# Performance work log

Hardware: AMD Instinct MI355X
Metric: run time of the kernel (lower is better)

Reference implementation:

```python
import math
import jax, jax.numpy as jnp
import numpy as np

B, L, D, H = 4, 512, 256, 8
DH = D // H
BUCKETS = 11  # rel_pos_buckets; padding_idx = BUCKETS


def setup_inputs() -> dict:
    key = jax.random.key(0)
    ks = jax.random.split(key, 12)
    s = 0.02
    rel_table = jax.random.normal(ks[10], (BUCKETS + 1, D), dtype=jnp.float32) * s
    rel_table = rel_table.at[BUCKETS].set(0.0)  # padding_idx row is zero
    return {
        "inputs": jax.random.normal(ks[0], (B, L, D), dtype=jnp.float32),
        "mask": jax.random.randint(ks[1], (B, L, L), 0, 2) > 0,
        "distances": jax.random.randint(ks[2], (B, L, L), 0, BUCKETS + 1),
        "Wq": jax.random.normal(ks[3], (D, D), dtype=jnp.float32) * s,
        "bq": jnp.zeros((D,), jnp.float32),
        "Wk": jax.random.normal(ks[4], (D, D), dtype=jnp.float32) * s,
        "bk": jnp.zeros((D,), jnp.float32),
        "Wv": jax.random.normal(ks[5], (D, D), dtype=jnp.float32) * s,
        "bv": jnp.zeros((D,), jnp.float32),
        "Wo": jax.random.normal(ks[6], (D, D), dtype=jnp.float32) * s,
        "bo": jnp.zeros((D,), jnp.float32),
        "rel_table": rel_table,
        "u": jax.random.normal(ks[7], (D,), dtype=jnp.float32) * s,
        "v": jax.random.normal(ks[8], (D,), dtype=jnp.float32) * s,
    }


def reference(inputs, mask, distances, Wq, bq, Wk, bk, Wv, bv, Wo, bo, rel_table, u, v):
    def shape(x):  # (B, L, D) -> (B, H, L, DH)
        return x.reshape(B, L, H, DH).transpose(0, 2, 1, 3)

    q = shape(inputs @ Wq + bq) / math.sqrt(DH)
    k = shape(inputs @ Wk + bk)
    val = shape(inputs @ Wv + bv)

    # content term: (q + u) k^T
    a_c = jnp.einsum("bhqd,bhkd->bhqk", q + u.reshape(1, H, 1, DH), k)

    # relative-position term: embedding gather (padding row already zero, mask anyway)
    valid = (distances != BUCKETS)[..., None].astype(rel_table.dtype)
    rel = (rel_table[distances] * valid).reshape(B, L, L, H, DH)  # (B, Lq, Lk, H, DH)
    b_d = jnp.einsum("bhqd,bqkhd->bhqk", q + v.reshape(1, H, 1, DH), rel)

    scores = jnp.where(mask[:, None, :, :], jnp.float32(-1e18), a_c + b_d)
    attn = jax.nn.softmax(scores, axis=-1)  # (B, H, Lq, Lk)

    ctx = jnp.einsum("bhqk,bhkd->bhqd", attn, val)
    ctx = ctx.transpose(0, 2, 1, 3).reshape(B, L, D)
    output = ctx @ Wo + bo
    return output, attn
```

## Files before the change

### kernel.cpp

```cpp
#include <hip/hip_runtime.h>
#include <math.h>

#define BB 4
#define LL 512
#define DD 256
#define HH 8
#define DHH 32
#define NB 12

__global__ __launch_bounds__(256) void qkv_kernel(const float* __restrict__ x,
    const float* __restrict__ Wq, const float* __restrict__ bq,
    const float* __restrict__ Wk, const float* __restrict__ bk,
    const float* __restrict__ Wv, const float* __restrict__ bv,
    const float* __restrict__ uvec, const float* __restrict__ vvec,
    float* __restrict__ Qu, float* __restrict__ Qv,
    float* __restrict__ KT, float* __restrict__ V) {
    __shared__ float xs[8][DD];
    const int mat = blockIdx.x >> 8;
    const int r0 = (blockIdx.x & 255) * 8;
    const int t = threadIdx.x;
    const int cg = t & 63, rg = t >> 6;
    const int c0 = cg * 4;
    {
        const float4* xg = (const float4*)(x + r0 * DD);
        float4* xsv = (float4*)&xs[0][0];
        xsv[t] = xg[t];
        xsv[t + 256] = xg[t + 256];
    }
    __syncthreads();
    const float* W    = (mat == 0) ? Wq : (mat == 1) ? Wk : Wv;
    const float* bias = (mat == 0) ? bq : (mat == 1) ? bk : bv;
    float acc[2][4];
#pragma unroll
    for (int r = 0; r < 2; ++r)
#pragma unroll
        for (int c = 0; c < 4; ++c) acc[r][c] = bias[c0 + c];
    for (int i0 = 0; i0 < DD; i0 += 4) {
        float4 wv4[4], xv4[2];
#pragma unroll
        for (int j = 0; j < 4; ++j) wv4[j] = *(const float4*)&W[(i0 + j) * DD + c0];
#pragma unroll
        for (int r = 0; r < 2; ++r) xv4[r] = *(const float4*)&xs[rg * 2 + r][i0];
        const float* wf = (const float*)wv4;
        const float* xf = (const float*)xv4;
#pragma unroll
        for (int r = 0; r < 2; ++r)
#pragma unroll
            for (int j = 0; j < 4; ++j)
#pragma unroll
                for (int c = 0; c < 4; ++c)
                    acc[r][c] = fmaf(xf[r * 4 + j], wf[j * 4 + c], acc[r][c]);
    }
    if (mat == 0) {
        const float s = 0.17677669529663687f;
        const float4 u4 = *(const float4*)&uvec[c0];
        const float4 v4 = *(const float4*)&vvec[c0];
#pragma unroll
        for (int r = 0; r < 2; ++r) {
            const int row = r0 + rg * 2 + r;
            float4 q = make_float4(acc[r][0] * s, acc[r][1] * s, acc[r][2] * s, acc[r][3] * s);
            *(float4*)&Qu[row * DD + c0] = make_float4(q.x + u4.x, q.y + u4.y, q.z + u4.z, q.w + u4.w);
            *(float4*)&Qv[row * DD + c0] = make_float4(q.x + v4.x, q.y + v4.y, q.z + v4.z, q.w + v4.w);
        }
    } else if (mat == 1) {
        const int b = r0 >> 9;
        const int kb = (r0 & 511) + rg * 2;
#pragma unroll
        for (int c = 0; c < 4; ++c) {
            const int col = c0 + c;
            const int h = col >> 5, dd = col & 31;
            float* p = KT + ((long)((b * HH + h) * DHH + dd)) * LL + kb;
            p[0] = acc[0][c];
            p[1] = acc[1][c];
        }
    } else {
#pragma unroll
        for (int r = 0; r < 2; ++r)
            *(float4*)&V[(r0 + rg * 2 + r) * DD + c0] =
                make_float4(acc[r][0], acc[r][1], acc[r][2], acc[r][3]);
    }
}

__global__ __launch_bounds__(512, 4) void scores_ctx_kernel(const float* __restrict__ Qu,
    const float* __restrict__ Qv, const float* __restrict__ KT,
    const float* __restrict__ rel_table, const int* __restrict__ mask,
    const int* __restrict__ dist, const float* __restrict__ V,
    float* __restrict__ attn, float* __restrict__ ctx) {
    __shared__ float Qs[16][DHH];
    __shared__ float Qv8[16][DHH];
    __shared__ float rels[NB][DHH + 1];
    __shared__ float Ps[16][NB];
    __shared__ float Ss[16][4][132];
    __shared__ float Vs[DHH][133];
    const int blk = blockIdx.x;
    const int h = blk & 7;
    const int rest = blk >> 3;
    const int qt = rest & 31;
    const int b = rest >> 5;
    const int q0 = qt * 16;
    const int t = threadIdx.x;
    const int w = t >> 6, l = t & 63;

    {
        const int r = t >> 5, c = t & 31;
        Qs[r][c]  = Qu[(b * LL + q0 + r) * DD + h * DHH + c];
        Qv8[r][c] = Qv[(b * LL + q0 + r) * DD + h * DHH + c];
    }
    if (t < NB * DHH) {
        rels[t >> 5][t & 31] = rel_table[(t >> 5) * DD + h * DHH + (t & 31)];
    }
    __syncthreads();
    if (t < 16 * NB) {
        const int bk = t >> 4, r = t & 15;
        float a = 0.f;
#pragma unroll
        for (int d = 0; d < DHH; ++d) a = fmaf(Qv8[r][d], rels[bk][d], a);
        Ps[r][bk] = a;
    }
    __syncthreads();

    const int r0 = 2 * w;
    const long kbase = (long)(b * HH + h) * DHH * LL;
    float e0[2][4], e1[2][4];
    float sum0 = 0.f, sum1 = 0.f;
#pragma unroll
    for (int s = 0; s < 2; ++s) {
        const int k0 = 4 * l + 256 * s;
        const int4 dx0 = *(const int4*)&dist[(b * LL + q0 + r0) * LL + k0];
        const int4 dx1 = *(const int4*)&dist[(b * LL + q0 + r0 + 1) * LL + k0];
        const int4 mx0 = *(const int4*)&mask[(b * LL + q0 + r0) * LL + k0];
        const int4 mx1 = *(const int4*)&mask[(b * LL + q0 + r0 + 1) * LL + k0];
        float s0[4], s1[4];
        s0[0] = Ps[r0][dx0.x]; s0[1] = Ps[r0][dx0.y]; s0[2] = Ps[r0][dx0.z]; s0[3] = Ps[r0][dx0.w];
        s1[0] = Ps[r0 + 1][dx1.x]; s1[1] = Ps[r0 + 1][dx1.y]; s1[2] = Ps[r0 + 1][dx1.z]; s1[3] = Ps[r0 + 1][dx1.w];
#pragma unroll
        for (int d8 = 0; d8 < DHH; d8 += 8) {
            float4 kv[8];
#pragma unroll
            for (int j = 0; j < 8; ++j)
                kv[j] = *(const float4*)&KT[kbase + (long)(d8 + j) * LL + k0];
            const float4 q0a = *(const float4*)&Qs[r0][d8];
            const float4 q0b = *(const float4*)&Qs[r0][d8 + 4];
            const float4 q1a = *(const float4*)&Qs[r0 + 1][d8];
            const float4 q1b = *(const float4*)&Qs[r0 + 1][d8 + 4];
            const float* qa0 = (const float*)&q0a;
            const float* qb0 = (const float*)&q0b;
            const float* qa1 = (const float*)&q1a;
            const float* qb1 = (const float*)&q1b;
#pragma unroll
            for (int j = 0; j < 4; ++j) {
                s0[0] = fmaf(qa0[j], kv[j].x, s0[0]);
                s0[1] = fmaf(qa0[j], kv[j].y, s0[1]);
                s0[2] = fmaf(qa0[j], kv[j].z, s0[2]);
                s0[3] = fmaf(qa0[j], kv[j].w, s0[3]);
                s1[0] = fmaf(qa1[j], kv[j].x, s1[0]);
                s1[1] = fmaf(qa1[j], kv[j].y, s1[1]);
                s1[2] = fmaf(qa1[j], kv[j].z, s1[2]);
                s1[3] = fmaf(qa1[j], kv[j].w, s1[3]);
            }
#pragma unroll
            for (int j = 0; j < 4; ++j) {
                s0[0] = fmaf(qb0[j], kv[j + 4].x, s0[0]);
                s0[1] = fmaf(qb0[j], kv[j + 4].y, s0[1]);
                s0[2] = fmaf(qb0[j], kv[j + 4].z, s0[2]);
                s0[3] = fmaf(qb0[j], kv[j + 4].w, s0[3]);
                s1[0] = fmaf(qb1[j], kv[j + 4].x, s1[0]);
                s1[1] = fmaf(qb1[j], kv[j + 4].y, s1[1]);
                s1[2] = fmaf(qb1[j], kv[j + 4].z, s1[2]);
                s1[3] = fmaf(qb1[j], kv[j + 4].w, s1[3]);
            }
        }
        e0[s][0] = mx0.x ? 0.f : __expf(s0[0]);
        e0[s][1] = mx0.y ? 0.f : __expf(s0[1]);
        e0[s][2] = mx0.z ? 0.f : __expf(s0[2]);
        e0[s][3] = mx0.w ? 0.f : __expf(s0[3]);
        e1[s][0] = mx1.x ? 0.f : __expf(s1[0]);
        e1[s][1] = mx1.y ? 0.f : __expf(s1[1]);
        e1[s][2] = mx1.z ? 0.f : __expf(s1[2]);
        e1[s][3] = mx1.w ? 0.f : __expf(s1[3]);
        sum0 += (e0[s][0] + e0[s][1]) + (e0[s][2] + e0[s][3]);
        sum1 += (e1[s][0] + e1[s][1]) + (e1[s][2] + e1[s][3]);
    }
    for (int off = 32; off > 0; off >>= 1) {
        sum0 += __shfl_xor(sum0, off);
        sum1 += __shfl_xor(sum1, off);
    }
    const float i0 = 1.0f / sum0, i1 = 1.0f / sum1;
    float* a0 = attn + ((long)(b * HH + h) * LL + q0 + r0) * LL;
    float* a1 = a0 + LL;
#pragma unroll
    for (int s = 0; s < 2; ++s) {
        const int k0 = 4 * l + 256 * s;
        const int ch = k0 >> 7, off = k0 & 127;
        const float4 o0 = make_float4(e0[s][0] * i0, e0[s][1] * i0, e0[s][2] * i0, e0[s][3] * i0);
        const float4 o1 = make_float4(e1[s][0] * i1, e1[s][1] * i1, e1[s][2] * i1, e1[s][3] * i1);
        *(float4*)&a0[k0] = o0;
        *(float4*)&a1[k0] = o1;
        *(float4*)&Ss[r0][ch][off] = o0;
        *(float4*)&Ss[r0 + 1][ch][off] = o1;
    }

    const int qB = t >> 5;
    const int dB = t & 31;
    const int kkS = t >> 2;
    const int dqS = (t & 3) * 8;
    float acc = 0.f;
    for (int c = 0; c < 4; ++c) {
        __syncthreads();
        {
            const float* vg = V + ((long)(b * LL + c * 128 + kkS)) * DD + h * DHH + dqS;
            const float4 va = *(const float4*)&vg[0];
            const float4 vb4 = *(const float4*)&vg[4];
            Vs[dqS + 0][kkS] = va.x;  Vs[dqS + 1][kkS] = va.y;
            Vs[dqS + 2][kkS] = va.z;  Vs[dqS + 3][kkS] = va.w;
            Vs[dqS + 4][kkS] = vb4.x; Vs[dqS + 5][kkS] = vb4.y;
            Vs[dqS + 6][kkS] = vb4.z; Vs[dqS + 7][kkS] = vb4.w;
        }
        __syncthreads();
#pragma unroll
        for (int j = 0; j < 32; ++j) {
            const float4 sv = *(const float4*)&Ss[qB][c][4 * j];
            const float4 vv = *(const float4*)&Vs[dB][4 * j];
            acc = fmaf(sv.x, vv.x, fmaf(sv.y, vv.y, fmaf(sv.z, vv.z, fmaf(sv.w, vv.w, acc))));
        }
    }
    ctx[(b * LL + q0 + qB) * DD + h * DHH + dB] = acc;
}

__global__ __launch_bounds__(256) void outproj_kernel(const float* __restrict__ ctx,
    const float* __restrict__ Wo, const float* __restrict__ bo,
    float* __restrict__ out) {
    __shared__ float xs[4][DD];
    const int r0 = blockIdx.x * 4;
    const int t = threadIdx.x;
    const int rg = t >> 6;
    const int c0 = (t & 63) * 4;
    ((float4*)&xs[0][0])[t] = ((const float4*)(ctx + r0 * DD))[t];
    __syncthreads();
    float4 acc = *(const float4*)&bo[c0];
    for (int i0 = 0; i0 < DD; i0 += 8) {
        float4 wv[8];
#pragma unroll
        for (int j = 0; j < 8; ++j) wv[j] = *(const float4*)&Wo[(i0 + j) * DD + c0];
        const float4 x0 = *(const float4*)&xs[rg][i0];
        const float4 x1 = *(const float4*)&xs[rg][i0 + 4];
        const float* xf0 = (const float*)&x0;
        const float* xf1 = (const float*)&x1;
#pragma unroll
        for (int j = 0; j < 4; ++j) {
            acc.x = fmaf(xf0[j], wv[j].x, acc.x);
            acc.y = fmaf(xf0[j], wv[j].y, acc.y);
            acc.z = fmaf(xf0[j], wv[j].z, acc.z);
            acc.w = fmaf(xf0[j], wv[j].w, acc.w);
        }
#pragma unroll
        for (int j = 0; j < 4; ++j) {
            acc.x = fmaf(xf1[j], wv[j + 4].x, acc.x);
            acc.y = fmaf(xf1[j], wv[j + 4].y, acc.y);
            acc.z = fmaf(xf1[j], wv[j + 4].z, acc.z);
            acc.w = fmaf(xf1[j], wv[j + 4].w, acc.w);
        }
    }
    *(float4*)&out[(r0 + rg) * DD + c0] = acc;
}

extern "C" void kernel_launch(void* const* d_in, const int* in_sizes, int n_in,
                              void* d_out, int out_size, void* d_ws, size_t ws_size,
                              hipStream_t stream) {
    const float* x    = (const float*)d_in[0];
    const int* mk     = (const int*)d_in[1];
    const int* dist   = (const int*)d_in[2];
    const float* Wq = (const float*)d_in[3];
    const float* bq = (const float*)d_in[4];
    const float* Wk = (const float*)d_in[5];
    const float* bk = (const float*)d_in[6];
    const float* Wv = (const float*)d_in[7];
    const float* bv = (const float*)d_in[8];
    const float* Wo = (const float*)d_in[9];
    const float* bo = (const float*)d_in[10];
    const float* rel_table = (const float*)d_in[11];
    const float* uvec = (const float*)d_in[12];
    const float* vvec = (const float*)d_in[13];

    float* out  = (float*)d_out;
    float* attn = out + BB * LL * DD;

    float* Qu = (float*)d_ws;
    float* Qv = Qu + BB * LL * DD;
    float* KT = Qv + BB * LL * DD;
    float* V  = KT + BB * LL * DD;
    float* C  = V + BB * LL * DD;

    qkv_kernel<<<3 * 256, 256, 0, stream>>>(x, Wq, bq, Wk, bk, Wv, bv, uvec, vvec,
                                            Qu, Qv, KT, V);
    scores_ctx_kernel<<<BB * (LL / 16) * HH, 512, 0, stream>>>(Qu, Qv, KT, rel_table,
                                                               mk, dist, V, attn, C);
    outproj_kernel<<<BB * LL / 4, 256, 0, stream>>>(C, Wo, bo, out);
}
```

Measured before the change: 179.8 us.

## Assign one key per thread across all query rows and widen QKV k-step

The scores kernel now has each thread own one key column, holding its 32-element K vector in registers and computing all 16 query rows. The previous scheme reloaded K tiles for every pair of rows per wave. The softmax row sums now use a cross-wave reduction through shared memory with an extra barrier. Masked entries become -1e30 before the exp instead of being zeroed afterwards. Separately, the QKV projection loop is unrolled to consume 8 input elements per iteration, raising register use in exchange for more loads in flight.

```diff
diff --git a/kernel.cpp b/kernel.cpp
--- a/kernel.cpp
+++ b/kernel.cpp
@@ -35,21 +35,30 @@
     for (int r = 0; r < 2; ++r)
 #pragma unroll
         for (int c = 0; c < 4; ++c) acc[r][c] = bias[c0 + c];
-    for (int i0 = 0; i0 < DD; i0 += 4) {
-        float4 wv4[4], xv4[2];
-#pragma unroll
-        for (int j = 0; j < 4; ++j) wv4[j] = *(const float4*)&W[(i0 + j) * DD + c0];
-#pragma unroll
-        for (int r = 0; r < 2; ++r) xv4[r] = *(const float4*)&xs[rg * 2 + r][i0];
-        const float* wf = (const float*)wv4;
-        const float* xf = (const float*)xv4;
-#pragma unroll
-        for (int r = 0; r < 2; ++r)
+    for (int i0 = 0; i0 < DD; i0 += 8) {
+        float4 wv4[8], xa[2], xb[2];
+#pragma unroll
+        for (int j = 0; j < 8; ++j) wv4[j] = *(const float4*)&W[(i0 + j) * DD + c0];
+#pragma unroll
+        for (int r = 0; r < 2; ++r) {
+            xa[r] = *(const float4*)&xs[rg * 2 + r][i0];
+            xb[r] = *(const float4*)&xs[rg * 2 + r][i0 + 4];
+        }
+#pragma unroll
+        for (int r = 0; r < 2; ++r) {
+            const float* xf = (const float*)&xa[r];
+            const float* xg2 = (const float*)&xb[r];
 #pragma unroll
             for (int j = 0; j < 4; ++j)
 #pragma unroll
                 for (int c = 0; c < 4; ++c)
-                    acc[r][c] = fmaf(xf[r * 4 + j], wf[j * 4 + c], acc[r][c]);
+                    acc[r][c] = fmaf(xf[j], ((const float*)&wv4[j])[c], acc[r][c]);
+#pragma unroll
+            for (int j = 0; j < 4; ++j)
+#pragma unroll
+                for (int c = 0; c < 4; ++c)
+                    acc[r][c] = fmaf(xg2[j], ((const float*)&wv4[j + 4])[c], acc[r][c]);
+        }
     }
     if (mat == 0) {
         const float s = 0.17677669529663687f;
@@ -90,6 +99,7 @@
     __shared__ float Qv8[16][DHH];
     __shared__ float rels[NB][DHH + 1];
     __shared__ float Ps[16][NB];
+    __shared__ float wsum[16][8];
     __shared__ float Ss[16][4][132];
     __shared__ float Vs[DHH][133];
     const int blk = blockIdx.x;
@@ -119,85 +129,55 @@
     }
     __syncthreads();
 
-    const int r0 = 2 * w;
-    const long kbase = (long)(b * HH + h) * DHH * LL;
-    float e0[2][4], e1[2][4];
-    float sum0 = 0.f, sum1 = 0.f;
-#pragma unroll
-    for (int s = 0; s < 2; ++s) {
-        const int k0 = 4 * l + 256 * s;
-        const int4 dx0 = *(const int4*)&dist[(b * LL + q0 + r0) * LL + k0];
-        const int4 dx1 = *(const int4*)&dist[(b * LL + q0 + r0 + 1) * LL + k0];
-        const int4 mx0 = *(const int4*)&mask[(b * LL + q0 + r0) * LL + k0];
-        const int4 mx1 = *(const int4*)&mask[(b * LL + q0 + r0 + 1) * LL + k0];
-        float s0[4], s1[4];
-        s0[0] = Ps[r0][dx0.x]; s0[1] = Ps[r0][dx0.y]; s0[2] = Ps[r0][dx0.z]; s0[3] = Ps[r0][dx0.w];
-        s1[0] = Ps[r0 + 1][dx1.x]; s1[1] = Ps[r0 + 1][dx1.y]; s1[2] = Ps[r0 + 1][dx1.z]; s1[3] = Ps[r0 + 1][dx1.w];
-#pragma unroll
-        for (int d8 = 0; d8 < DHH; d8 += 8) {
-            float4 kv[8];
-#pragma unroll
-            for (int j = 0; j < 8; ++j)
-                kv[j] = *(const float4*)&KT[kbase + (long)(d8 + j) * LL + k0];
-            const float4 q0a = *(const float4*)&Qs[r0][d8];
-            const float4 q0b = *(const float4*)&Qs[r0][d8 + 4];
-            const float4 q1a = *(const float4*)&Qs[r0 + 1][d8];
-            const float4 q1b = *(const float4*)&Qs[r0 + 1][d8 + 4];
-            const float* qa0 = (const float*)&q0a;
-            const float* qb0 = (const float*)&q0b;
-            const float* qa1 = (const float*)&q1a;
-            const float* qb1 = (const float*)&q1b;
-#pragma unroll
-            for (int j = 0; j < 4; ++j) {
-                s0[0] = fmaf(qa0[j], kv[j].x, s0[0]);
-                s0[1] = fmaf(qa0[j], kv[j].y, s0[1]);
-                s0[2] = fmaf(qa0[j], kv[j].z, s0[2]);
-                s0[3] = fmaf(qa0[j], kv[j].w, s0[3]);
-                s1[0] = fmaf(qa1[j], kv[j].x, s1[0]);
-                s1[1] = fmaf(qa1[j], kv[j].y, s1[1]);
-                s1[2] = fmaf(qa1[j], kv[j].z, s1[2]);
-                s1[3] = fmaf(qa1[j], kv[j].w, s1[3]);
+    float kd[DHH];
+    {
+        const float* ktp = KT + (long)(b * HH + h) * DHH * LL + t;
+#pragma unroll
+        for (int j = 0; j < DHH; ++j) kd[j] = ktp[(long)j * LL];
+    }
+    float e[16];
+    {
+        float base[16];
+#pragma unroll
+        for (int r = 0; r < 16; ++r) {
+            const int mq = (b * LL + q0 + r) * LL + t;
+            const int dv = dist[mq];
+            const int mv = mask[mq];
+            base[r] = mv ? -1e30f : Ps[r][dv];
+        }
+#pragma unroll
+        for (int r = 0; r < 16; ++r) {
+            float acc = base[r];
+            const float4* qup = (const float4*)&Qs[r][0];
+#pragma unroll
+            for (int j = 0; j < 8; ++j) {
+                const float4 qq = qup[j];
+                acc = fmaf(qq.x, kd[4 * j + 0], acc);
+                acc = fmaf(qq.y, kd[4 * j + 1], acc);
+                acc = fmaf(qq.z, kd[4 * j + 2], acc);
+                acc = fmaf(qq.w, kd[4 * j + 3], acc);
             }
-#pragma unroll
-            for (int j = 0; j < 4; ++j) {
-                s0[0] = fmaf(qb0[j], kv[j + 4].x, s0[0]);
-                s0[1] = fmaf(qb0[j], kv[j + 4].y, s0[1]);
-                s0[2] = fmaf(qb0[j], kv[j + 4].z, s0[2]);
-                s0[3] = fmaf(qb0[j], kv[j + 4].w, s0[3]);
-                s1[0] = fmaf(qb1[j], kv[j + 4].x, s1[0]);
-                s1[1] = fmaf(qb1[j], kv[j + 4].y, s1[1]);
-                s1[2] = fmaf(qb1[j], kv[j + 4].z, s1[2]);
-                s1[3] = fmaf(qb1[j], kv[j + 4].w, s1[3]);
-            }
-        }
-        e0[s][0] = mx0.x ? 0.f : __expf(s0[0]);
-        e0[s][1] = mx0.y ? 0.f : __expf(s0[1]);
-        e0[s][2] = mx0.z ? 0.f : __expf(s0[2]);
-        e0[s][3] = mx0.w ? 0.f : __expf(s0[3]);
-        e1[s][0] = mx1.x ? 0.f : __expf(s1[0]);
-        e1[s][1] = mx1.y ? 0.f : __expf(s1[1]);
-        e1[s][2] = mx1.z ? 0.f : __expf(s1[2]);
-        e1[s][3] = mx1.w ? 0.f : __expf(s1[3]);
-        sum0 += (e0[s][0] + e0[s][1]) + (e0[s][2] + e0[s][3]);
-        sum1 += (e1[s][0] + e1[s][1]) + (e1[s][2] + e1[s][3]);
-    }
-    for (int off = 32; off > 0; off >>= 1) {
-        sum0 += __shfl_xor(sum0, off);
-        sum1 += __shfl_xor(sum1, off);
-    }
-    const float i0 = 1.0f / sum0, i1 = 1.0f / sum1;
-    float* a0 = attn + ((long)(b * HH + h) * LL + q0 + r0) * LL;
-    float* a1 = a0 + LL;
-#pragma unroll
-    for (int s = 0; s < 2; ++s) {
-        const int k0 = 4 * l + 256 * s;
-        const int ch = k0 >> 7, off = k0 & 127;
-        const float4 o0 = make_float4(e0[s][0] * i0, e0[s][1] * i0, e0[s][2] * i0, e0[s][3] * i0);
-        const float4 o1 = make_float4(e1[s][0] * i1, e1[s][1] * i1, e1[s][2] * i1, e1[s][3] * i1);
-        *(float4*)&a0[k0] = o0;
-        *(float4*)&a1[k0] = o1;
-        *(float4*)&Ss[r0][ch][off] = o0;
-        *(float4*)&Ss[r0 + 1][ch][off] = o1;
+            e[r] = __expf(acc);
+        }
+    }
+#pragma unroll
+    for (int r = 0; r < 16; ++r) {
+        float s = e[r];
+        for (int off = 32; off > 0; off >>= 1) s += __shfl_xor(s, off);
+        if (l == 0) wsum[r][w] = s;
+    }
+    __syncthreads();
+    const int chA = t >> 7, offA = t & 127;
+    float* ag = attn + ((long)(b * HH + h) * LL + q0) * LL + t;
+#pragma unroll
+    for (int r = 0; r < 16; ++r) {
+        const float4 s0 = *(const float4*)&wsum[r][0];
+        const float4 s1 = *(const float4*)&wsum[r][4];
+        const float inv = 1.0f / ((s0.x + s0.y + s0.z + s0.w) +
+                                  (s1.x + s1.y + s1.z + s1.w));
+        const float a = e[r] * inv;
+        ag[(long)r * LL] = a;
+        Ss[r][chA][offA] = a;
     }
 
     const int qB = t >> 5;
```

Measured after the change: 583.0 us. 224% more time.
